# Performance work log

Measured on AMD Instinct MI355X. Metric: run time of the kernel, lower is better.

## Reference

```python
import jax, jax.numpy as jnp
import numpy as np

N = 8388608  # number of neurons


def spu(x):
    # SPU(x) = x^2 - 0.5 for x >= 0, sigmoid(-x) - 1 for x < 0
    return jnp.where(x >= 0, x * x - 0.5, jax.nn.sigmoid(-x) - 1.0)


def setup_inputs() -> dict:
    key = jax.random.key(0)
    k1, k2, k3, k4, k5, k6 = jax.random.split(key, 6)
    c = jax.random.normal(k1, (N,), dtype=jnp.float32)
    w = jax.random.uniform(k2, (N,), dtype=jnp.float32, minval=0.01, maxval=1.0)
    bounds = jnp.stack([c - w, c + w], axis=1)  # strictly lower < upper
    cp = jax.random.normal(k3, (N,), dtype=jnp.float32)
    wp = jax.random.uniform(k4, (N,), dtype=jnp.float32, minval=0.01, maxval=1.0)
    bounds_prev = jnp.stack([cp - wp, cp + wp], axis=1)
    slopes_prev = 0.5 * jax.random.normal(k5, (N, 2), dtype=jnp.float32)
    shifts_prev = 0.5 * jax.random.normal(k6, (N, 2), dtype=jnp.float32)
    return {"bounds": bounds, "slopes_prev": slopes_prev,
            "shifts_prev": shifts_prev, "bounds_prev": bounds_prev}


def reference(bounds, slopes_prev, shifts_prev, bounds_prev):
    l, u = bounds[:, 0], bounds[:, 1]
    sl, su = spu(l), spu(u)
    neg = u <= 0
    pos = l >= 0
    cross = jnp.logical_not(jnp.logical_or(neg, pos))
    all_slopes = (su - sl) / (u - l)
    # box=False: upper slope set on pos and cross, lower slope set on neg
    s0 = jnp.where(neg, all_slopes, 0.0)              # slopes[:, 0]
    s1 = jnp.where(pos | cross, all_slopes, 0.0)       # slopes[:, 1]
    # bounds = spu(bounds), swap where all_slopes < 0, cross lower = -0.5
    neg_slope = all_slopes < 0
    lo = jnp.where(neg_slope, su, sl)
    hi = jnp.where(neg_slope, sl, su)
    lo = jnp.where(cross, -0.5, lo)
    # shifts
    sh1 = su - s1 * u
    sh0 = sl - s0 * l
    sh0 = jnp.where(cross, -0.5, sh0)
    sh1 = jnp.where(neg, sl, sh1)
    # ---- back_sub (steps_backsub=2) ----
    # top layer: upper_Matrix = diag(s1), lower_Matrix = diag(s0),
    # upper_Vector = sh1, lower_Vector = sh0.
    # All matmuls in back_sub_from_top_layer are diag@diag or diag@vec, so
    # they reduce exactly to elementwise products (identical math, O(n)).
    p1l, p1u = slopes_prev[:, 0], slopes_prev[:, 1]
    q1l, q1u = shifts_prev[:, 0], shifts_prev[:, 1]
    s1p, s1n = jnp.maximum(s1, 0.0), jnp.minimum(s1, 0.0)
    s0p, s0n = jnp.maximum(s0, 0.0), jnp.minimum(s0, 0.0)
    UBM = s1p * p1u + s1n * p1l   # diag of Upper_Boundary_Matrix
    UBV = s1p * q1u + sh1 + s1n * q1l
    LBM = s0p * p1l + s0n * p1u   # diag of Lower_Boundary_Matrix
    LBV = s0n * q1l + sh0 + s0p * q1u
    b0l, b0u = bounds_prev[:, 0], bounds_prev[:, 1]
    lower = jnp.maximum(LBM, 0.0) * b0l + jnp.minimum(LBM, 0.0) * b0u + LBV
    upper = jnp.maximum(UBM, 0.0) * b0u + jnp.minimum(UBM, 0.0) * b0l + UBV
    # merge back-substituted bounds where they are tighter
    lo = jnp.where(lower > lo, lower, lo)
    hi = jnp.where(upper < hi, upper, hi)
    return jnp.stack([lo, hi], axis=1)
```

## Files before the change

kernel.cpp:

```cpp
#include <hip/hip_runtime.h>
#include <math.h>


typedef float nfloat4 __attribute__((ext_vector_type(4)));

__device__ __forceinline__ float spu_f(float x) {
    if (x >= 0.0f) {
        return x * x - 0.5f;
    } else {
        return 1.0f / (1.0f + __expf(x)) - 1.0f;
    }
}

__device__ __forceinline__ void spu_row(float l, float u,
                                        float p1l, float p1u,
                                        float q1l, float q1u,
                                        float b0l, float b0u,
                                        float& out_lo, float& out_hi) {
    const float sl = spu_f(l);
    const float su = spu_f(u);

    const bool neg   = (u <= 0.0f);
    const bool pos   = (l >= 0.0f);
    const bool cross = !(neg || pos);

    const float all_slopes = (su - sl) / (u - l);

    const float s0 = neg ? all_slopes : 0.0f;
    const float s1 = (pos || cross) ? all_slopes : 0.0f;

    const bool neg_slope = (all_slopes < 0.0f);
    float lo = neg_slope ? su : sl;
    float hi = neg_slope ? sl : su;
    lo = cross ? -0.5f : lo;

    float sh1 = fmaf(-s1, u, su);
    float sh0 = fmaf(-s0, l, sl);
    sh0 = cross ? -0.5f : sh0;
    sh1 = neg ? sl : sh1;

    const float s1p = fmaxf(s1, 0.0f), s1n = fminf(s1, 0.0f);
    const float s0p = fmaxf(s0, 0.0f), s0n = fminf(s0, 0.0f);

    const float UBM = s1p * p1u + s1n * p1l;
    const float UBV = s1p * q1u + sh1 + s1n * q1l;
    const float LBM = s0p * p1l + s0n * p1u;
    const float LBV = s0n * q1l + sh0 + s0p * q1u;

    const float lower = fmaxf(LBM, 0.0f) * b0l + fminf(LBM, 0.0f) * b0u + LBV;
    const float upper = fmaxf(UBM, 0.0f) * b0u + fminf(UBM, 0.0f) * b0l + UBV;

    out_lo = (lower > lo) ? lower : lo;
    out_hi = (upper < hi) ? upper : hi;
}

__device__ __forceinline__ nfloat4 spu_quad(const nfloat4 b, const nfloat4 sp,
                                            const nfloat4 sh, const nfloat4 bp) {
    float o0, o1, o2, o3;
    spu_row(b.x, b.y, sp.x, sp.y, sh.x, sh.y, bp.x, bp.y, o0, o1);
    spu_row(b.z, b.w, sp.z, sp.w, sh.z, sh.w, bp.z, bp.w, o2, o3);
    nfloat4 o;
    o.x = o0; o.y = o1; o.z = o2; o.w = o3;
    return o;
}

__global__ __launch_bounds__(256) void SPUTransformer_62002147885333_kernel(
    const nfloat4* __restrict__ bounds,
    const nfloat4* __restrict__ slopes_prev,
    const nfloat4* __restrict__ shifts_prev,
    const nfloat4* __restrict__ bounds_prev,
    nfloat4* __restrict__ out,
    int npairs)
{
    const int i = blockIdx.x * blockDim.x + threadIdx.x;
    if (i < npairs) {
        const nfloat4 b  = __builtin_nontemporal_load(&bounds[i]);
        const nfloat4 sp = __builtin_nontemporal_load(&slopes_prev[i]);
        const nfloat4 sh = __builtin_nontemporal_load(&shifts_prev[i]);
        const nfloat4 bp = __builtin_nontemporal_load(&bounds_prev[i]);

        const nfloat4 o = spu_quad(b, sp, sh, bp);

        __builtin_nontemporal_store(o, &out[i]);
    }
}

extern "C" void kernel_launch(void* const* d_in, const int* in_sizes, int n_in,
                              void* d_out, int out_size, void* d_ws, size_t ws_size,
                              hipStream_t stream) {
    const nfloat4* bounds      = (const nfloat4*)d_in[0];
    const nfloat4* slopes_prev = (const nfloat4*)d_in[1];
    const nfloat4* shifts_prev = (const nfloat4*)d_in[2];
    const nfloat4* bounds_prev = (const nfloat4*)d_in[3];
    nfloat4* out = (nfloat4*)d_out;

    const int n_rows = in_sizes[0] / 2;
    const int npairs = n_rows / 2;

    const int block = 256;
    const int grid = (npairs + block - 1) / block;

    SPUTransformer_62002147885333_kernel<<<grid, block, 0, stream>>>(
        bounds, slopes_prev, shifts_prev, bounds_prev, out, npairs);
}
```

Before: 235.1 us.

## Use grid-stride loop with software-prefetched next-iteration loads

Replaces the one-element-per-thread launch with a fixed 2048-block grid-stride loop. Each thread issues the loads for its next element before computing and storing the current one. The goal is to keep more memory requests in flight per thread and to cut block launch overhead on a purely bandwidth-bound kernel. In exchange, the fixed grid may lower occupancy-driven parallelism, and the doubled live registers may hurt occupancy.

```diff
diff --git a/kernel.cpp b/kernel.cpp
--- a/kernel.cpp
+++ b/kernel.cpp
@@ -70,18 +70,35 @@
     const nfloat4* __restrict__ shifts_prev,
     const nfloat4* __restrict__ bounds_prev,
     nfloat4* __restrict__ out,
-    int npairs)
+    int nquads)
 {
-    const int i = blockIdx.x * blockDim.x + threadIdx.x;
-    if (i < npairs) {
-        const nfloat4 b  = __builtin_nontemporal_load(&bounds[i]);
-        const nfloat4 sp = __builtin_nontemporal_load(&slopes_prev[i]);
-        const nfloat4 sh = __builtin_nontemporal_load(&shifts_prev[i]);
-        const nfloat4 bp = __builtin_nontemporal_load(&bounds_prev[i]);
+    const int stride = gridDim.x * blockDim.x;
+    int i = blockIdx.x * blockDim.x + threadIdx.x;
+    if (i >= nquads) return;
+
+    nfloat4 b  = __builtin_nontemporal_load(&bounds[i]);
+    nfloat4 sp = __builtin_nontemporal_load(&slopes_prev[i]);
+    nfloat4 sh = __builtin_nontemporal_load(&shifts_prev[i]);
+    nfloat4 bp = __builtin_nontemporal_load(&bounds_prev[i]);
+
+    while (true) {
+        const int inext = i + stride;
+        const bool have_next = (inext < nquads);
+
+        nfloat4 bn, spn, shn, bpn;
+        if (have_next) {
+            bn  = __builtin_nontemporal_load(&bounds[inext]);
+            spn = __builtin_nontemporal_load(&slopes_prev[inext]);
+            shn = __builtin_nontemporal_load(&shifts_prev[inext]);
+            bpn = __builtin_nontemporal_load(&bounds_prev[inext]);
+        }
 
         const nfloat4 o = spu_quad(b, sp, sh, bp);
+        __builtin_nontemporal_store(o, &out[i]);
 
-        __builtin_nontemporal_store(o, &out[i]);
+        if (!have_next) break;
+        b = bn; sp = spn; sh = shn; bp = bpn;
+        i = inext;
     }
 }
 
@@ -95,11 +112,13 @@
     nfloat4* out = (nfloat4*)d_out;
 
     const int n_rows = in_sizes[0] / 2;
-    const int npairs = n_rows / 2;
+    const int nquads = n_rows / 2;
 
     const int block = 256;
-    const int grid = (npairs + block - 1) / block;
+    int grid = 2048;
+    const long long needed = ((long long)nquads + block - 1) / block;
+    if ((long long)grid > needed) grid = (int)needed;
 
     SPUTransformer_62002147885333_kernel<<<grid, block, 0, stream>>>(
-        bounds, slopes_prev, shifts_prev, bounds_prev, out, npairs);
+        bounds, slopes_prev, shifts_prev, bounds_prev, out, nquads);
 }
```

Result: no change. 238.5 us (+1.4%).
